# Performance work log

Measured on AMD Instinct MI355X. Metric: run time of the kernel, lower is better.

Reference implementation:

```python
import jax, jax.numpy as jnp
from jax import lax
import numpy as np

_B, _D, _H, _W = 4, 32, 256, 256   # batch, sparse grid (z,y,x)
_NPER = 50000                      # active voxels per batch element
_EPS = 1e-3                        # BatchNorm eps from norm_fn


def _subm_rulebook(coords, D, H, W):
    # gather/scatter index pairs for a 3x3x3 submanifold conv (spconv rulebook)
    N = coords.shape[0]
    b, z, y, x = coords.T
    keys = ((b * D + z) * H + y) * W + x
    order = np.argsort(keys)
    sk = keys[order]
    rin, rout = [], []
    for dz in (-1, 0, 1):
        for dy in (-1, 0, 1):
            for dx in (-1, 0, 1):
                nz, ny, nx = z + dz, y + dy, x + dx
                valid = (nz >= 0) & (nz < D) & (ny >= 0) & (ny < H) & (nx >= 0) & (nx < W)
                qk = ((b * D + nz) * H + ny) * W + nx
                pos = np.clip(np.searchsorted(sk, qk), 0, N - 1)
                found = valid & (sk[pos] == qk)
                rin.append(order[pos[found]].astype(np.int32))
                rout.append(np.nonzero(found)[0].astype(np.int32))
    P = max(len(a) for a in rin)
    Ia = np.full((27, P), N, np.int32)   # sentinel N -> zero-padded row
    Oa = np.full((27, P), N, np.int32)
    for k in range(27):
        Ia[k, :len(rin[k])] = rin[k]
        Oa[k, :len(rout[k])] = rout[k]
    return Ia, Oa


def _build():
    rng = np.random.default_rng(0)
    coords = []
    for b in range(_B):
        lin = rng.choice(_D * _H * _W, _NPER, replace=False)
        z = lin // (_H * _W); y = (lin // _W) % _H; x = lin % _W
        coords.append(np.stack([np.full(_NPER, b), z, y, x], 1))
    coords = np.concatenate(coords).astype(np.int64)
    N = coords.shape[0]
    rb1_in, rb1_out = _subm_rulebook(coords, _D, _H, _W)
    # strided SparseConv3d (k=3, s=2, p=1) rulebook + output coord set
    Do, Ho, Wo = (_D - 1) // 2 + 1, (_H - 1) // 2 + 1, (_W - 1) // 2 + 1
    b, z, y, x = coords.T
    cin, ck, ckey = [], [], []
    k = 0
    for dz in range(3):
        for dy in range(3):
            for dx in range(3):
                oz2, oy2, ox2 = z + 1 - dz, y + 1 - dy, x + 1 - dx
                valid = (oz2 % 2 == 0) & (oy2 % 2 == 0) & (ox2 % 2 == 0)
                oz, oy, ox = oz2 // 2, oy2 // 2, ox2 // 2
                valid &= (oz >= 0) & (oz < Do) & (oy >= 0) & (oy < Ho) & (ox >= 0) & (ox < Wo)
                idx = np.nonzero(valid)[0]
                cin.append(idx)
                ck.append(np.full(len(idx), k))
                ckey.append(((b[idx] * Do + oz[idx]) * Ho + oy[idx]) * Wo + ox[idx])
                k += 1
    allkey = np.concatenate(ckey)
    ukeys, inv = np.unique(allkey, return_inverse=True)
    N2 = len(ukeys)
    cin = np.concatenate(cin); ck = np.concatenate(ck)
    Pd = max(int((ck == kk).sum()) for kk in range(27))
    Id = np.full((27, Pd), N, np.int32)
    Od = np.full((27, Pd), N2, np.int32)
    for kk in range(27):
        m = ck == kk; n = int(m.sum())
        Id[kk, :n] = cin[m]; Od[kk, :n] = inv[m]
    ox = ukeys % Wo; oy = (ukeys // Wo) % Ho
    oz = (ukeys // (Wo * Ho)) % Do; ob = ukeys // (Wo * Ho * Do)
    coords2 = np.stack([ob, oz, oy, ox], 1)
    rb2_in, rb2_out = _subm_rulebook(coords2, Do, Ho, Wo)
    return N, N2, rb1_in, rb1_out, Id, Od, rb2_in, rb2_out


def setup_inputs():
    N, N2, rb1_in, rb1_out, rbd_in, rbd_out, rb2_in, rb2_out = _build()
    ks = jax.random.split(jax.random.key(0), 8)
    Cin, C0, C1 = 5, 16, 32
    return dict(
        voxel_features=jax.random.normal(ks[0], (N, Cin), jnp.float32),
        W_in=jax.random.normal(ks[1], (27, Cin, C0), jnp.float32) * 0.1,
        g_in=jnp.ones(C0), b_in=jnp.zeros(C0),
        Wb1=jax.random.normal(ks[2], (2, 2, 27, C0, C0), jnp.float32) * 0.05,
        bb1=jnp.zeros((2, 2, C0)), gb1=jnp.ones((2, 2, C0)), beb1=jnp.zeros((2, 2, C0)),
        Wp=jax.random.normal(ks[3], (27, C0, 1), jnp.float32) * 0.05,
        Wd=jax.random.normal(ks[4], (27, C0, C1), jnp.float32) * 0.05,
        g_d=jnp.ones(C1), b_d=jnp.zeros(C1),
        Wb2=jax.random.normal(ks[5], (2, 2, 27, C1, C1), jnp.float32) * 0.05,
        bb2=jnp.zeros((2, 2, C1)), gb2=jnp.ones((2, 2, C1)), beb2=jnp.zeros((2, 2, C1)),
        rb1_in=jnp.asarray(rb1_in), rb1_out=jnp.asarray(rb1_out),
        rbd_in=jnp.asarray(rbd_in), rbd_out=jnp.asarray(rbd_out),
        rb2_in=jnp.asarray(rb2_in), rb2_out=jnp.asarray(rb2_out),
        n2=int(N2),
    )


def _sparse_conv(feat, W, rin, rout, nout):
    # rulebook gather-matmul-scatter; fixed 27-iteration loop over kernel offsets
    featp = jnp.concatenate([feat, jnp.zeros((1, feat.shape[1]), feat.dtype)], 0)
    out = jnp.zeros((nout + 1, W.shape[-1]), feat.dtype)
    for k in range(W.shape[0]):
        out = out.at[rout[k]].add(featp[rin[k]] @ W[k])
    return out[:nout]


def _bn(x, g, b):
    # training-mode BatchNorm1d over active voxels (eps=1e-3)
    m = x.mean(0)
    v = ((x - m) ** 2).mean(0)
    return g * (x - m) * lax.rsqrt(v + _EPS) + b


def _basic_block(feat, Wb, bb, gb, beb, rin, rout, n):
    out = _sparse_conv(feat, Wb[0], rin, rout, n) + bb[0]
    out = jax.nn.relu(_bn(out, gb[0], beb[0]))
    out = _sparse_conv(out, Wb[1], rin, rout, n) + bb[1]
    out = _bn(out, gb[1], beb[1])
    return jax.nn.relu(out + feat)


def _forward(voxel_features, W_in, g_in, b_in, Wb1, bb1, gb1, beb1, Wp, Wd, g_d, b_d,
             Wb2, bb2, gb2, beb2, rb1_in, rb1_out, rbd_in, rbd_out, rb2_in, rb2_out, n2):
    n1 = voxel_features.shape[0]
    # conv_input: SubMConv3d + BN + ReLU
    x = jax.nn.relu(_bn(_sparse_conv(voxel_features, W_in, rb1_in, rb1_out, n1), g_in, b_in))
    for i in range(2):
        x = _basic_block(x, Wb1[i], bb1[i], gb1[i], beb1[i], rb1_in, rb1_out, n1)
    # DynamicFocalPruningDownsample: learnable importance -> topk keep (1-0.5)
    imp = jax.nn.sigmoid(_sparse_conv(x, Wp, rb1_in, rb1_out, n1))[:, 0]
    x = x * imp[:, None]
    kkeep = n1 - n1 // 2
    kth = lax.top_k(imp, kkeep)[0][-1]
    x = jnp.where(imp[:, None] >= kth, x, jnp.zeros_like(x))
    # strided SparseConv3d 16->32 + BN + ReLU
    x2 = jax.nn.relu(_bn(_sparse_conv(x, Wd, rbd_in, rbd_out, n2), g_d, b_d))
    for i in range(2):
        x2 = _basic_block(x2, Wb2[i], bb2[i], gb2[i], beb2[i], rb2_in, rb2_out, n2)
    return x2


def reference(voxel_features, W_in, g_in, b_in, Wb1, bb1, gb1, beb1, Wp, Wd, g_d, b_d,
              Wb2, bb2, gb2, beb2, rb1_in, rb1_out, rbd_in, rbd_out, rb2_in, rb2_out, n2):
    return _forward(voxel_features, W_in, g_in, b_in, Wb1, bb1, gb1, beb1, Wp, Wd, g_d, b_d,
                    Wb2, bb2, gb2, beb2, rb1_in, rb1_out, rbd_in, rbd_out, rb2_in, rb2_out, n2)
```

## Files before the change

kernel.cpp:

```cpp
#include <hip/hip_runtime.h>


typedef __attribute__((ext_vector_type(8))) short bf16x8;
typedef __attribute__((ext_vector_type(4))) float f32x4;

static __device__ __forceinline__ unsigned f2bfu(float x) {
    unsigned b = __float_as_uint(x);
    return (b + 0x7FFFu + ((b >> 16) & 1u)) >> 16;
}
static __device__ __forceinline__ float bf2f(unsigned short u) {
    return __uint_as_float(((unsigned)u) << 16);
}
static __device__ __forceinline__ int xcd_swz(int bid, int nwg) {
    if (nwg < 16) return bid;
    int q = nwg >> 3, r = nwg & 7;
    int x = bid & 7, i = bid >> 3;
    return (x < r ? x * (q + 1) : r * (q + 1) + (x - r) * q) + i;
}

__global__ void rb_count_kernel(const int* __restrict__ rout, int P, int n_out,
                                int* __restrict__ cnt) {
    int k = threadIdx.x;
    if (k >= 27) return;
    const int* r = rout + (size_t)k * P;
    int lo = 0, hi = P;
    while (lo < hi) {
        int mid = (lo + hi) >> 1;
        if (r[mid] < n_out) lo = mid + 1; else hi = mid;
    }
    cnt[k] = lo;
}

__global__ void seg_build(const int* __restrict__ rout, const int* __restrict__ cnt,
                          int P, int nb, int gran, int* __restrict__ segs) {
    const int k = blockIdx.y;
    const int b = blockIdx.x * 256 + threadIdx.x;
    if (b > nb) return;
    const int target = b * gran;
    const int* r = rout + (size_t)k * P;
    int lo = 0, hi = cnt[k];
    while (lo < hi) {
        int m = (lo + hi) >> 1;
        if (r[m] < target) lo = m + 1; else hi = m;
    }
    segs[k * (nb + 1) + b] = lo;
}

__global__ void inv_build(const int* __restrict__ rin, const int* __restrict__ rout,
                          const int* __restrict__ cnt, int P, int n_out,
                          int* __restrict__ inv) {
    const int k = blockIdx.y;
    const int p = blockIdx.x * 256 + threadIdx.x;
    if (p < cnt[k])
        inv[(size_t)k * n_out + rout[(size_t)k * P + p]] = rin[(size_t)k * P + p];
}

__global__ void prepack_w(const float* __restrict__ W, int T, int CI, int S,
                          short* __restrict__ pack) {
    int idx = blockIdx.x * 256 + threadIdx.x;
    if (idx >= S * 128) return;
    int l = idx & 63, h = (idx >> 6) & 1, s = idx >> 7;
    int co = (l & 15) + 16 * h;
#pragma unroll
    for (int j = 0; j < 8; j++) {
        int gk = s * 32 + (l >> 4) * 8 + j;
        int tap = gk / CI, cin = gk % CI;
        float w = (tap < T) ? W[((size_t)tap * CI + cin) * 32 + co] : 0.f;
        pack[(size_t)idx * 8 + j] = (short)f2bfu(w);
    }
}

template <bool OUT_BF16>
__global__ __launch_bounds__(256) void conv_mfma_sorted32(
        const unsigned short* __restrict__ feat, const short* __restrict__ Bp,
        const int* __restrict__ rin, const int* __restrict__ rout,
        const int* __restrict__ segs, int P, int nb16, int n_out,
        void* __restrict__ outv, float* __restrict__ stats) {
    __shared__ int invw[64];
    __shared__ float part[2][4][32];
    const int t = threadIdx.x, wv = t >> 6, lane = t & 63;
    const int row = lane & 15, grp = lane >> 4;
    const int bid = xcd_swz(blockIdx.x, gridDim.x);
    float ss0 = 0.f, qq0 = 0.f, ss1 = 0.f, qq1 = 0.f;

    for (int tile = 0; tile < 4; ++tile) {
        const int rowbase = bid * 256 + wv * 64 + tile * 16;
        if (rowbase >= n_out) break;
        const int tix = rowbase >> 4;
        int segv = 0;
        if (lane < 28)      segv = segs[lane * (nb16 + 1) + tix];
        else if (lane < 56) segv = segs[(lane - 28) * (nb16 + 1) + tix + 1];
        f32x4 d0 = {0.f, 0.f, 0.f, 0.f}, d1 = {0.f, 0.f, 0.f, 0.f};
        for (int k = 0; k < 27; ++k) {
            const int s0 = __shfl(segv, k);
            const int s1 = __shfl(segv, 28 + k);
            if (s0 == s1) continue;
            if (lane < 16) invw[wv * 16 + lane] = -1;
            const int e = s0 + lane;
            if (lane < 16 && e < s1)
                invw[wv * 16 + (rout[(size_t)k * P + e] - rowbase)] = rin[(size_t)k * P + e];
            asm volatile("s_waitcnt lgkmcnt(0)" ::: "memory");
            const int rn = invw[wv * 16 + row];
            union { int u[4]; bf16x8 v; } ua;
            ua.u[0] = ua.u[1] = ua.u[2] = ua.u[3] = 0;
            if (rn >= 0)
                ua.v = *(const bf16x8*)(feat + (size_t)rn * 32 + grp * 8);
            const bf16x8 b0 = *(const bf16x8*)(Bp + ((size_t)(2 * k) * 64 + lane) * 8);
            const bf16x8 b1 = *(const bf16x8*)(Bp + ((size_t)(2 * k + 1) * 64 + lane) * 8);
            d0 = __builtin_amdgcn_mfma_f32_16x16x32_bf16(ua.v, b0, d0, 0, 0, 0);
            d1 = __builtin_amdgcn_mfma_f32_16x16x32_bf16(ua.v, b1, d1, 0, 0, 0);
        }
        const int m0 = rowbase + grp * 4;
#pragma unroll
        for (int i = 0; i < 4; i++) {
            if (m0 + i < n_out) {
                if (OUT_BF16) {
                    unsigned short* o = (unsigned short*)outv;
                    o[(size_t)(m0 + i) * 32 + row]      = (unsigned short)f2bfu(d0[i]);
                    o[(size_t)(m0 + i) * 32 + row + 16] = (unsigned short)f2bfu(d1[i]);
                } else {
                    float* o = (float*)outv;
                    o[(size_t)(m0 + i) * 32 + row]      = d0[i];
                    o[(size_t)(m0 + i) * 32 + row + 16] = d1[i];
                }
            }
            ss0 += d0[i]; qq0 += d0[i] * d0[i];
            ss1 += d1[i]; qq1 += d1[i] * d1[i];
        }
    }
#pragma unroll
    for (int d = 16; d <= 32; d <<= 1) {
        ss0 += __shfl_xor(ss0, d); qq0 += __shfl_xor(qq0, d);
        ss1 += __shfl_xor(ss1, d); qq1 += __shfl_xor(qq1, d);
    }
    if (lane < 16) {
        part[0][wv][row] = ss0; part[0][wv][row + 16] = ss1;
        part[1][wv][row] = qq0; part[1][wv][row + 16] = qq1;
    }
    __syncthreads();
    if (t < 64) {
        const int which = t >> 5, co = t & 31;
        atomicAdd(&stats[which * 32 + co],
                  part[which][0][co] + part[which][1][co] +
                  part[which][2][co] + part[which][3][co]);
    }
}

__global__ __launch_bounds__(256) void conv_mfma_inv16(
        const unsigned short* __restrict__ feat, const short* __restrict__ Bp,
        const int* __restrict__ inv, int n_out,
        unsigned short* __restrict__ out, float* __restrict__ stats) {
    __shared__ float part[2][4][32];
    const int t = threadIdx.x, wv = t >> 6, lane = t & 63;
    const int row = lane & 15, grp = lane >> 4;
    const int bid = xcd_swz(blockIdx.x, gridDim.x);
    float ss0 = 0.f, qq0 = 0.f, ss1 = 0.f, qq1 = 0.f;

    for (int tile = 0; tile < 4; ++tile) {
        const int rowbase = bid * 256 + wv * 64 + tile * 16;
        if (rowbase >= n_out) break;
        const int j = rowbase + row;
        f32x4 d0 = {0.f, 0.f, 0.f, 0.f}, d1 = {0.f, 0.f, 0.f, 0.f};
        for (int s = 0; s < 14; ++s) {
            const int tap = 2 * s + (grp >> 1);
            const int cin0 = (grp & 1) * 8;
            int rn = -1;
            if (tap < 27 && j < n_out) rn = inv[(size_t)tap * n_out + j];
            union { int u[4]; bf16x8 v; } ua;
            ua.u[0] = ua.u[1] = ua.u[2] = ua.u[3] = 0;
            if (rn >= 0)
                ua.v = *(const bf16x8*)(feat + (size_t)rn * 16 + cin0);
            const bf16x8 b0 = *(const bf16x8*)(Bp + ((size_t)(2 * s) * 64 + lane) * 8);
            const bf16x8 b1 = *(const bf16x8*)(Bp + ((size_t)(2 * s + 1) * 64 + lane) * 8);
            d0 = __builtin_amdgcn_mfma_f32_16x16x32_bf16(ua.v, b0, d0, 0, 0, 0);
            d1 = __builtin_amdgcn_mfma_f32_16x16x32_bf16(ua.v, b1, d1, 0, 0, 0);
        }
        const int m0 = rowbase + grp * 4;
#pragma unroll
        for (int i = 0; i < 4; i++) {
            if (m0 + i < n_out) {
                out[(size_t)(m0 + i) * 32 + row]      = (unsigned short)f2bfu(d0[i]);
                out[(size_t)(m0 + i) * 32 + row + 16] = (unsigned short)f2bfu(d1[i]);
            }
            ss0 += d0[i]; qq0 += d0[i] * d0[i];
            ss1 += d1[i]; qq1 += d1[i] * d1[i];
        }
    }
#pragma unroll
    for (int d = 16; d <= 32; d <<= 1) {
        ss0 += __shfl_xor(ss0, d); qq0 += __shfl_xor(qq0, d);
        ss1 += __shfl_xor(ss1, d); qq1 += __shfl_xor(qq1, d);
    }
    if (lane < 16) {
        part[0][wv][row] = ss0; part[0][wv][row + 16] = ss1;
        part[1][wv][row] = qq0; part[1][wv][row + 16] = qq1;
    }
    __syncthreads();
    if (t < 64) {
        const int which = t >> 5, co = t & 31;
        atomicAdd(&stats[which * 32 + co],
                  part[which][0][co] + part[which][1][co] +
                  part[which][2][co] + part[which][3][co]);
    }
}

template <int COUT, bool SIGMOID, bool STATS>
__global__ __launch_bounds__(256) void conv16_wave(
        const float* __restrict__ feat, const float* __restrict__ W,
        const int* __restrict__ rin, const int* __restrict__ rout,
        const int* __restrict__ segs, int P, int nb64, int n_out,
        float* __restrict__ out, float* __restrict__ stats) {
    __shared__ int invw[4 * 64];
    __shared__ float part[2][4][COUT];
    const int t = threadIdx.x, wv = t >> 6, lane = t & 63;
    const int bid = xcd_swz(blockIdx.x, gridDim.x);
    const int rowbase = bid * 256 + wv * 64;
    const bool active = rowbase < n_out;
    float acc[COUT];
#pragma unroll
    for (int co = 0; co < COUT; co++) acc[co] = 0.f;

    if (active) {
        const int tix = rowbase >> 6;
        int segv = 0;
        if (lane < 28)      segv = segs[lane * (nb64 + 1) + tix];
        else if (lane < 56) segv = segs[(lane - 28) * (nb64 + 1) + tix + 1];
        for (int k = 0; k < 27; ++k) {
            const int s0 = __shfl(segv, k);
            const int s1 = __shfl(segv, 28 + k);
            if (s0 == s1) continue;
            invw[wv * 64 + lane] = -1;
            const int e = s0 + lane;
            if (e < s1)
                invw[wv * 64 + (rout[(size_t)k * P + e] - rowbase)] = rin[(size_t)k * P + e];
            asm volatile("s_waitcnt lgkmcnt(0)" ::: "memory");
            const int rn = invw[wv * 64 + lane];
            float f[16];
#pragma unroll
            for (int ci = 0; ci < 16; ci++) f[ci] = 0.f;
            if (rn >= 0) {
                const float* fr = feat + (size_t)rn * 16;
#pragma unroll
                for (int q = 0; q < 4; q++) {
                    const float4 v = *(const float4*)(fr + 4 * q);
                    f[4 * q] = v.x; f[4 * q + 1] = v.y;
                    f[4 * q + 2] = v.z; f[4 * q + 3] = v.w;
                }
            }
            const float* __restrict__ Wk = W + k * 16 * COUT;
#pragma unroll
            for (int ci = 0; ci < 16; ci++) {
                const float fv = f[ci];
#pragma unroll
                for (int co = 0; co < COUT; co++)
                    acc[co] = fmaf(fv, Wk[ci * COUT + co], acc[co]);
            }
        }
        const int j = rowbase + lane;
        if (j < n_out) {
#pragma unroll
            for (int co = 0; co < COUT; co++) {
                float v = acc[co];
                if (SIGMOID) v = 1.f / (1.f + expf(-v));
                out[(size_t)j * COUT + co] = v;
            }
        }
    }
    if (STATS) {
#pragma unroll
        for (int co = 0; co < COUT; co++) {
            float s = acc[co], s2 = s * s;
#pragma unroll
            for (int d = 1; d < 64; d <<= 1) {
                s += __shfl_xor(s, d);
                s2 += __shfl_xor(s2, d);
            }
            if (lane == 0) { part[0][wv][co] = s; part[1][wv][co] = s2; }
        }
        __syncthreads();
        if (t < 2 * COUT) {
            const int which = t / COUT, co = t - which * COUT;
            atomicAdd(&stats[which * COUT + co],
                      part[which][0][co] + part[which][1][co] +
                      part[which][2][co] + part[which][3][co]);
        }
    }
}

template <int CIN, int COUT>
__global__ __launch_bounds__(256) void conv_gather(
        const float* __restrict__ feat, const float* __restrict__ W,
        const int* __restrict__ rin, const int* __restrict__ rout,
        const int* __restrict__ segs, int P, int n_out,
        float* __restrict__ out, float* __restrict__ stats) {
    __shared__ int2 invl[256];
    __shared__ int seg[54];
    __shared__ float part[2][4][COUT];
    const int t = threadIdx.x;
    const int bid = xcd_swz(blockIdx.x, gridDim.x);
    const int j0 = bid * 256;
    const int nb1 = gridDim.x + 1;
    if (t < 54) seg[t] = segs[(t >> 1) * nb1 + bid + (t & 1)];
    invl[t] = make_int2(-1, -1);
    float acc[COUT];
#pragma unroll
    for (int co = 0; co < COUT; co++) acc[co] = 0.f;
    __syncthreads();

    for (int k = 0; k < 27; k++) {
        const int s0 = seg[2 * k], s1 = seg[2 * k + 1];
        if (s0 == s1) continue;
        const int idx = s0 + t;
        if (idx < s1)
            invl[rout[(size_t)k * P + idx] - j0] = make_int2(k, rin[(size_t)k * P + idx]);
        __syncthreads();
        const int2 e = invl[t];
        const int in = (e.x == k) ? e.y : -1;
        __syncthreads();

        float f[CIN];
#pragma unroll
        for (int ci = 0; ci < CIN; ci++) f[ci] = 0.f;
        if (in >= 0) {
            const float* fr = feat + (size_t)in * CIN;
#pragma unroll
            for (int ci = 0; ci < CIN; ci++) f[ci] = fr[ci];
        }
        const float* __restrict__ Wk = W + k * CIN * COUT;
#pragma unroll
        for (int ci = 0; ci < CIN; ci++) {
            const float fv = f[ci];
#pragma unroll
            for (int co = 0; co < COUT; co++)
                acc[co] = fmaf(fv, Wk[ci * COUT + co], acc[co]);
        }
    }

    const int j = j0 + t;
    if (j < n_out) {
#pragma unroll
        for (int co = 0; co < COUT; co++) out[(size_t)j * COUT + co] = acc[co];
    }
    const int wv = t >> 6, lane = t & 63;
#pragma unroll
    for (int co = 0; co < COUT; co++) {
        float s = acc[co], s2 = s * s;
#pragma unroll
        for (int d = 1; d < 64; d <<= 1) {
            s += __shfl_xor(s, d);
            s2 += __shfl_xor(s2, d);
        }
        if (lane == 0) { part[0][wv][co] = s; part[1][wv][co] = s2; }
    }
    __syncthreads();
    if (t < 2 * COUT) {
        const int which = t / COUT, co = t - which * COUT;
        atomicAdd(&stats[which * COUT + co],
                  part[which][0][co] + part[which][1][co] +
                  part[which][2][co] + part[which][3][co]);
    }
}

template <int C, bool RELU>
__global__ void bn_apply(const float* __restrict__ x, const float* __restrict__ stats,
                         const float* __restrict__ gg, const float* __restrict__ bb,
                         int n, float* __restrict__ y) {
    const float nf = (float)n;
    const long long total = (long long)n * C;
    for (long long idx = (long long)blockIdx.x * blockDim.x + threadIdx.x;
         idx < total; idx += (long long)gridDim.x * blockDim.x) {
        int ch = (int)(idx & (C - 1));
        float m = stats[ch] / nf;
        float v = stats[C + ch] / nf - m * m;
        float r = rsqrtf(v + 1e-3f);
        float val = gg[ch] * (x[idx] - m) * r + bb[ch];
        if (RELU) val = fmaxf(val, 0.f);
        y[idx] = val;
    }
}

template <int C>
__global__ void bn_apply_addrelu(const float* __restrict__ x,
                                 const float* __restrict__ skip,
                                 const float* __restrict__ stats,
                                 const float* __restrict__ gg,
                                 const float* __restrict__ bb,
                                 int n, float* __restrict__ y) {
    const float nf = (float)n;
    const long long total = (long long)n * C;
    for (long long idx = (long long)blockIdx.x * blockDim.x + threadIdx.x;
         idx < total; idx += (long long)gridDim.x * blockDim.x) {
        int ch = (int)(idx & (C - 1));
        float m = stats[ch] / nf;
        float v = stats[C + ch] / nf - m * m;
        float r = rsqrtf(v + 1e-3f);
        float val = gg[ch] * (x[idx] - m) * r + bb[ch] + skip[idx];
        y[idx] = fmaxf(val, 0.f);
    }
}

template <int C>
__global__ void bn_apply_b(const unsigned short* __restrict__ x,
                           const float* __restrict__ stats,
                           const float* __restrict__ gg, const float* __restrict__ bb,
                           int n, unsigned short* __restrict__ y) {
    const float nf = (float)n;
    const long long total = (long long)n * C;
    for (long long idx = (long long)blockIdx.x * blockDim.x + threadIdx.x;
         idx < total; idx += (long long)gridDim.x * blockDim.x) {
        int ch = (int)(idx & (C - 1));
        float m = stats[ch] / nf;
        float v = stats[C + ch] / nf - m * m;
        float r = rsqrtf(v + 1e-3f);
        float val = gg[ch] * (bf2f(x[idx]) - m) * r + bb[ch];
        val = fmaxf(val, 0.f);
        y[idx] = (unsigned short)f2bfu(val);
    }
}

template <int C, bool OUT_BF16>
__global__ void bn_addrelu_sb(const float* __restrict__ x,
                              const unsigned short* __restrict__ skip,
                              const float* __restrict__ stats,
                              const float* __restrict__ gg,
                              const float* __restrict__ bb,
                              int n, void* __restrict__ yv) {
    const float nf = (float)n;
    const long long total = (long long)n * C;
    for (long long idx = (long long)blockIdx.x * blockDim.x + threadIdx.x;
         idx < total; idx += (long long)gridDim.x * blockDim.x) {
        int ch = (int)(idx & (C - 1));
        float m = stats[ch] / nf;
        float v = stats[C + ch] / nf - m * m;
        float r = rsqrtf(v + 1e-3f);
        float val = gg[ch] * (x[idx] - m) * r + bb[ch] + bf2f(skip[idx]);
        val = fmaxf(val, 0.f);
        if (OUT_BF16) ((unsigned short*)yv)[idx] = (unsigned short)f2bfu(val);
        else          ((float*)yv)[idx] = val;
    }
}

__global__ __launch_bounds__(256) void hist_pass(const float* __restrict__ imp, int n,
                                                 int pass, const int* __restrict__ state,
                                                 int* __restrict__ hist) {
    __shared__ int lh[256];
    const int t = threadIdx.x;
    lh[t] = 0;
    __syncthreads();
    const int shift = 24 - 8 * pass;
    unsigned prefix = 0;
    if (pass > 0) prefix = (unsigned)state[0];
    for (int i = blockIdx.x * 256 + t; i < n; i += gridDim.x * 256) {
        unsigned u = __float_as_uint(imp[i]);
        if (pass == 0 || (u >> (shift + 8)) == prefix)
            atomicAdd(&lh[(u >> shift) & 0xFFu], 1);
    }
    __syncthreads();
    if (lh[t]) atomicAdd(&hist[pass * 256 + t], lh[t]);
}

__global__ __launch_bounds__(256) void scan_byte(const int* __restrict__ hist,
                                                 int kkeep, int pass,
                                                 int* __restrict__ state) {
    __shared__ int h[256];
    const int t = threadIdx.x;
    h[t] = hist[pass * 256 + t];
    __syncthreads();
    if (t == 0) {
        const int target = (pass == 0) ? kkeep : state[1];
        int acc = 0; int b = 255;
        for (; b > 0; b--) {
            if (acc + h[b] >= target) break;
            acc += h[b];
        }
        unsigned prefix = (pass == 0) ? 0u : (unsigned)state[0];
        prefix = (prefix << 8) | (unsigned)b;
        state[0] = (int)prefix;
        state[1] = target - acc;
        if (pass == 3) state[2] = (int)prefix;
    }
}

__global__ void prune_mask_ab(const float* __restrict__ x, const float* __restrict__ imp,
                              const int* __restrict__ state, int n,
                              unsigned short* __restrict__ ab) {
    const unsigned K = (unsigned)state[2];
    int i = blockIdx.x * blockDim.x + threadIdx.x;
    if (i >= n) return;
    float im = imp[i];
    float mult = (__float_as_uint(im) >= K) ? im : 0.f;
#pragma unroll
    for (int c = 0; c < 16; c++)
        ab[(size_t)i * 16 + c] = (unsigned short)f2bfu(x[(size_t)i * 16 + c] * mult);
}

extern "C" void kernel_launch(void* const* d_in, const int* in_sizes, int n_in,
                              void* d_out, int out_size, void* d_ws, size_t ws_size,
                              hipStream_t stream) {
    const float* vf    = (const float*)d_in[0];
    const float* W_in  = (const float*)d_in[1];
    const float* g_in  = (const float*)d_in[2];
    const float* b_in  = (const float*)d_in[3];
    const float* Wb1   = (const float*)d_in[4];
    const float* gb1   = (const float*)d_in[6];
    const float* beb1  = (const float*)d_in[7];
    const float* Wp    = (const float*)d_in[8];
    const float* Wd    = (const float*)d_in[9];
    const float* g_d   = (const float*)d_in[10];
    const float* b_d   = (const float*)d_in[11];
    const float* Wb2   = (const float*)d_in[12];
    const float* gb2   = (const float*)d_in[14];
    const float* beb2  = (const float*)d_in[15];
    const int* rb1_in  = (const int*)d_in[16];
    const int* rb1_out = (const int*)d_in[17];
    const int* rbd_in  = (const int*)d_in[18];
    const int* rbd_out = (const int*)d_in[19];
    const int* rb2_in  = (const int*)d_in[20];
    const int* rb2_out = (const int*)d_in[21];

    const int N  = in_sizes[0] / 5;
    const int P1 = in_sizes[16] / 27;
    const int Pd = in_sizes[18] / 27;
    const int P2 = in_sizes[20] / 27;
    const int n2 = out_size / 32;
    const int kkeep = N - N / 2;

    const int gs1   = (N + 255) / 256;
    const int gm2   = (n2 + 255) / 256;
    const int nb16  = (n2 + 15) / 16;
    const int nb64  = (N + 63) / 64;
    const int gew   = 2048;

    auto pad4 = [](size_t v) { return (v + 3) & ~(size_t)3; };
    float* A     = (float*)d_ws;
    float* B     = A   + pad4((size_t)N * 16);
    float* imp   = B   + pad4((size_t)N * 16);
    float* FI    = imp + pad4((size_t)N);
    float* Dbf   = FI  + pad4((size_t)n2 * 32);
    float* Ebf   = Dbf + pad4((size_t)n2 * 16);
    float* stats = Ebf + pad4((size_t)n2 * 16);
    int*   cnt1  = (int*)(stats + 64);
    int*   cntd  = cnt1 + 32;
    int*   cnt2  = cntd + 32;
    int*   hist4 = cnt2 + 32;
    int*   state = hist4 + 1024;
    int*   segs1 = state + 8;
    int*   segs64 = segs1 + 27 * (gs1 + 1);
    int*   invd   = (int*)FI;
    float* F      = FI;
    unsigned short* Ab = (unsigned short*)B;
    int*   segs16 = (int*)(B + pad4((size_t)N * 8));
    short* pack2  = (short*)imp;
    short* packd  = pack2 + 4 * 27648;
    unsigned short* Db = (unsigned short*)Dbf;
    unsigned short* Eb = (unsigned short*)Ebf;
    float* OUT   = (float*)d_out;
    float* C2    = OUT;

    rb_count_kernel<<<1, 32, 0, stream>>>(rb1_out, P1, N,  cnt1);
    rb_count_kernel<<<1, 32, 0, stream>>>(rbd_out, Pd, n2, cntd);
    rb_count_kernel<<<1, 32, 0, stream>>>(rb2_out, P2, n2, cnt2);
    seg_build<<<dim3((gs1 + 256) / 256, 27), 256, 0, stream>>>(rb1_out, cnt1, P1, gs1, 256, segs1);
    seg_build<<<dim3((nb64 + 256) / 256, 27), 256, 0, stream>>>(rb1_out, cnt1, P1, nb64, 64, segs64);

    hipMemsetAsync(stats, 0, 64 * 4, stream);
    conv_gather<5, 16><<<gs1, 256, 0, stream>>>(vf, W_in, rb1_in, rb1_out, segs1, P1, N, B, stats);
    bn_apply<16, true><<<gew, 256, 0, stream>>>(B, stats, g_in, b_in, N, A);

    for (int i = 0; i < 2; i++) {
        const float* W0 = Wb1 + (size_t)(i * 2 + 0) * 27 * 256;
        const float* W1 = Wb1 + (size_t)(i * 2 + 1) * 27 * 256;
        hipMemsetAsync(stats, 0, 64 * 4, stream);
        conv16_wave<16, false, true><<<gs1, 256, 0, stream>>>(A, W0, rb1_in, rb1_out, segs64, P1, nb64, N, B, stats);
        bn_apply<16, true><<<gew, 256, 0, stream>>>(B, stats, gb1 + (i * 2 + 0) * 16, beb1 + (i * 2 + 0) * 16, N, B);
        hipMemsetAsync(stats, 0, 64 * 4, stream);
        conv16_wave<16, false, true><<<gs1, 256, 0, stream>>>(B, W1, rb1_in, rb1_out, segs64, P1, nb64, N, C2, stats);
        bn_apply_addrelu<16><<<gew, 256, 0, stream>>>(C2, A, stats, gb1 + (i * 2 + 1) * 16, beb1 + (i * 2 + 1) * 16, N, A);
    }

    conv16_wave<1, true, false><<<gs1, 256, 0, stream>>>(A, Wp, rb1_in, rb1_out, segs64, P1, nb64, N, imp, stats);
    hipMemsetAsync(hist4, 0, 1024 * 4, stream);
    for (int p = 0; p < 4; p++) {
        hist_pass<<<128, 256, 0, stream>>>(imp, N, p, state, hist4);
        scan_byte<<<1, 256, 0, stream>>>(hist4, kkeep, p, state);
    }
    prune_mask_ab<<<(N + 255) / 256, 256, 0, stream>>>(A, imp, state, N, Ab);

    seg_build<<<dim3((nb16 + 256) / 256, 27), 256, 0, stream>>>(rb2_out, cnt2, P2, nb16, 16, segs16);
    for (int w = 0; w < 4; w++)
        prepack_w<<<14, 256, 0, stream>>>(Wb2 + (size_t)w * 27 * 1024, 27, 32, 27, pack2 + (size_t)w * 27648);
    prepack_w<<<7, 256, 0, stream>>>(Wd, 27, 16, 14, packd);
    hipMemsetAsync(invd, 0xFF, (size_t)27 * n2 * 4, stream);
    inv_build<<<dim3((Pd + 255) / 256, 27), 256, 0, stream>>>(rbd_in, rbd_out, cntd, Pd, n2, invd);

    hipMemsetAsync(stats, 0, 64 * 4, stream);
    conv_mfma_inv16<<<gm2, 256, 0, stream>>>(Ab, packd, invd, n2, Db, stats);
    bn_apply_b<32><<<gew, 256, 0, stream>>>(Db, stats, g_d, b_d, n2, Db);

    for (int i = 0; i < 2; i++) {
        const short* P0 = pack2 + (size_t)(i * 2 + 0) * 27648;
        const short* P1w = pack2 + (size_t)(i * 2 + 1) * 27648;
        hipMemsetAsync(stats, 0, 64 * 4, stream);
        conv_mfma_sorted32<true><<<gm2, 256, 0, stream>>>(Db, P0, rb2_in, rb2_out, segs16, P2, nb16, n2, Eb, stats);
        bn_apply_b<32><<<gew, 256, 0, stream>>>(Eb, stats, gb2 + (i * 2 + 0) * 32, beb2 + (i * 2 + 0) * 32, n2, Eb);
        hipMemsetAsync(stats, 0, 64 * 4, stream);
        conv_mfma_sorted32<false><<<gm2, 256, 0, stream>>>(Eb, P1w, rb2_in, rb2_out, segs16, P2, nb16, n2, F, stats);
        if (i == 0)
            bn_addrelu_sb<32, true><<<gew, 256, 0, stream>>>(F, Db, stats, gb2 + 32, beb2 + 32, n2, Db);
        else
            bn_addrelu_sb<32, false><<<gew, 256, 0, stream>>>(F, Db, stats, gb2 + 96, beb2 + 96, n2, OUT);
    }
}
```

Measured before the change: 1.282 ms.

## Replace segment-sorted rulebook gather with dense inverse index for 32ch convs

```diff
diff --git a/kernel.cpp b/kernel.cpp
--- a/kernel.cpp
+++ b/kernel.cpp
@@ -71,12 +71,10 @@
 }
 
 template <bool OUT_BF16>
-__global__ __launch_bounds__(256) void conv_mfma_sorted32(
+__global__ __launch_bounds__(256, 4) void conv_mfma_inv32(
         const unsigned short* __restrict__ feat, const short* __restrict__ Bp,
-        const int* __restrict__ rin, const int* __restrict__ rout,
-        const int* __restrict__ segs, int P, int nb16, int n_out,
+        const int* __restrict__ inv, int n_out,
         void* __restrict__ outv, float* __restrict__ stats) {
-    __shared__ int invw[64];
     __shared__ float part[2][4][32];
     const int t = threadIdx.x, wv = t >> 6, lane = t & 63;
     const int row = lane & 15, grp = lane >> 4;
@@ -86,21 +84,12 @@
     for (int tile = 0; tile < 4; ++tile) {
         const int rowbase = bid * 256 + wv * 64 + tile * 16;
         if (rowbase >= n_out) break;
-        const int tix = rowbase >> 4;
-        int segv = 0;
-        if (lane < 28)      segv = segs[lane * (nb16 + 1) + tix];
-        else if (lane < 56) segv = segs[(lane - 28) * (nb16 + 1) + tix + 1];
+        const int j = rowbase + row;
+        const bool jv = j < n_out;
         f32x4 d0 = {0.f, 0.f, 0.f, 0.f}, d1 = {0.f, 0.f, 0.f, 0.f};
+#pragma unroll
         for (int k = 0; k < 27; ++k) {
-            const int s0 = __shfl(segv, k);
-            const int s1 = __shfl(segv, 28 + k);
-            if (s0 == s1) continue;
-            if (lane < 16) invw[wv * 16 + lane] = -1;
-            const int e = s0 + lane;
-            if (lane < 16 && e < s1)
-                invw[wv * 16 + (rout[(size_t)k * P + e] - rowbase)] = rin[(size_t)k * P + e];
-            asm volatile("s_waitcnt lgkmcnt(0)" ::: "memory");
-            const int rn = invw[wv * 16 + row];
+            const int rn = jv ? inv[(size_t)k * n_out + j] : -1;
             union { int u[4]; bf16x8 v; } ua;
             ua.u[0] = ua.u[1] = ua.u[2] = ua.u[3] = 0;
             if (rn >= 0)
@@ -146,7 +135,7 @@
     }
 }
 
-__global__ __launch_bounds__(256) void conv_mfma_inv16(
+__global__ __launch_bounds__(256, 4) void conv_mfma_inv16(
         const unsigned short* __restrict__ feat, const short* __restrict__ Bp,
         const int* __restrict__ inv, int n_out,
         unsigned short* __restrict__ out, float* __restrict__ stats) {
@@ -160,12 +149,14 @@
         const int rowbase = bid * 256 + wv * 64 + tile * 16;
         if (rowbase >= n_out) break;
         const int j = rowbase + row;
+        const bool jv = j < n_out;
         f32x4 d0 = {0.f, 0.f, 0.f, 0.f}, d1 = {0.f, 0.f, 0.f, 0.f};
+#pragma unroll
         for (int s = 0; s < 14; ++s) {
             const int tap = 2 * s + (grp >> 1);
             const int cin0 = (grp & 1) * 8;
             int rn = -1;
-            if (tap < 27 && j < n_out) rn = inv[(size_t)tap * n_out + j];
+            if (tap < 27 && jv) rn = inv[(size_t)tap * n_out + j];
             union { int u[4]; bf16x8 v; } ua;
             ua.u[0] = ua.u[1] = ua.u[2] = ua.u[3] = 0;
             if (rn >= 0)
@@ -418,13 +409,13 @@
     }
 }
 
-template <int C, bool OUT_BF16>
-__global__ void bn_addrelu_sb(const float* __restrict__ x,
-                              const unsigned short* __restrict__ skip,
-                              const float* __restrict__ stats,
-                              const float* __restrict__ gg,
-                              const float* __restrict__ bb,
-                              int n, void* __restrict__ yv) {
+template <int C, bool XBF16, bool OUT_BF16>
+__global__ void bn_addrelu_x(const void* __restrict__ xv,
+                             const unsigned short* __restrict__ skip,
+                             const float* __restrict__ stats,
+                             const float* __restrict__ gg,
+                             const float* __restrict__ bb,
+                             int n, void* __restrict__ yv) {
     const float nf = (float)n;
     const long long total = (long long)n * C;
     for (long long idx = (long long)blockIdx.x * blockDim.x + threadIdx.x;
@@ -433,7 +424,9 @@
         float m = stats[ch] / nf;
         float v = stats[C + ch] / nf - m * m;
         float r = rsqrtf(v + 1e-3f);
-        float val = gg[ch] * (x[idx] - m) * r + bb[ch] + bf2f(skip[idx]);
+        float x = XBF16 ? bf2f(((const unsigned short*)xv)[idx])
+                        : ((const float*)xv)[idx];
+        float val = gg[ch] * (x - m) * r + bb[ch] + bf2f(skip[idx]);
         val = fmaxf(val, 0.f);
         if (OUT_BF16) ((unsigned short*)yv)[idx] = (unsigned short)f2bfu(val);
         else          ((float*)yv)[idx] = val;
@@ -527,7 +520,6 @@
 
     const int gs1   = (N + 255) / 256;
     const int gm2   = (n2 + 255) / 256;
-    const int nb16  = (n2 + 15) / 16;
     const int nb64  = (N + 63) / 64;
     const int gew   = 2048;
 
@@ -535,8 +527,8 @@
     float* A     = (float*)d_ws;
     float* B     = A   + pad4((size_t)N * 16);
     float* imp   = B   + pad4((size_t)N * 16);
-    float* FI    = imp + pad4((size_t)N);
-    float* Dbf   = FI  + pad4((size_t)n2 * 32);
+    float* INVf  = imp + pad4((size_t)N);
+    float* Dbf   = INVf + pad4((size_t)n2 * 27);
     float* Ebf   = Dbf + pad4((size_t)n2 * 16);
     float* stats = Ebf + pad4((size_t)n2 * 16);
     int*   cnt1  = (int*)(stats + 64);
@@ -546,15 +538,14 @@
     int*   state = hist4 + 1024;
     int*   segs1 = state + 8;
     int*   segs64 = segs1 + 27 * (gs1 + 1);
-    int*   invd   = (int*)FI;
-    float* F      = FI;
+    int*   INV    = (int*)INVf;
     unsigned short* Ab = (unsigned short*)B;
-    int*   segs16 = (int*)(B + pad4((size_t)N * 8));
     short* pack2  = (short*)imp;
     short* packd  = pack2 + 4 * 27648;
     unsigned short* Db = (unsigned short*)Dbf;
     unsigned short* Eb = (unsigned short*)Ebf;
     float* OUT   = (float*)d_out;
+    unsigned short* OUTb = (unsigned short*)d_out;
     float* C2    = OUT;
 
     rb_count_kernel<<<1, 32, 0, stream>>>(rb1_out, P1, N,  cnt1);
@@ -586,28 +577,32 @@
     }
     prune_mask_ab<<<(N + 255) / 256, 256, 0, stream>>>(A, imp, state, N, Ab);
 
-    seg_build<<<dim3((nb16 + 256) / 256, 27), 256, 0, stream>>>(rb2_out, cnt2, P2, nb16, 16, segs16);
     for (int w = 0; w < 4; w++)
         prepack_w<<<14, 256, 0, stream>>>(Wb2 + (size_t)w * 27 * 1024, 27, 32, 27, pack2 + (size_t)w * 27648);
     prepack_w<<<7, 256, 0, stream>>>(Wd, 27, 16, 14, packd);
-    hipMemsetAsync(invd, 0xFF, (size_t)27 * n2 * 4, stream);
-    inv_build<<<dim3((Pd + 255) / 256, 27), 256, 0, stream>>>(rbd_in, rbd_out, cntd, Pd, n2, invd);
+    hipMemsetAsync(INV, 0xFF, (size_t)27 * n2 * 4, stream);
+    inv_build<<<dim3((Pd + 255) / 256, 27), 256, 0, stream>>>(rbd_in, rbd_out, cntd, Pd, n2, INV);
 
     hipMemsetAsync(stats, 0, 64 * 4, stream);
-    conv_mfma_inv16<<<gm2, 256, 0, stream>>>(Ab, packd, invd, n2, Db, stats);
+    conv_mfma_inv16<<<gm2, 256, 0, stream>>>(Ab, packd, INV, n2, Db, stats);
     bn_apply_b<32><<<gew, 256, 0, stream>>>(Db, stats, g_d, b_d, n2, Db);
+
+    hipMemsetAsync(INV, 0xFF, (size_t)27 * n2 * 4, stream);
+    inv_build<<<dim3((P2 + 255) / 256, 27), 256, 0, stream>>>(rb2_in, rb2_out, cnt2, P2, n2, INV);
 
     for (int i = 0; i < 2; i++) {
         const short* P0 = pack2 + (size_t)(i * 2 + 0) * 27648;
         const short* P1w = pack2 + (size_t)(i * 2 + 1) * 27648;
         hipMemsetAsync(stats, 0, 64 * 4, stream);
-        conv_mfma_sorted32<true><<<gm2, 256, 0, stream>>>(Db, P0, rb2_in, rb2_out, segs16, P2, nb16, n2, Eb, stats);
+        conv_mfma_inv32<true><<<gm2, 256, 0, stream>>>(Db, P0, INV, n2, Eb, stats);
         bn_apply_b<32><<<gew, 256, 0, stream>>>(Eb, stats, gb2 + (i * 2 + 0) * 32, beb2 + (i * 2 + 0) * 32, n2, Eb);
         hipMemsetAsync(stats, 0, 64 * 4, stream);
-        conv_mfma_sorted32<false><<<gm2, 256, 0, stream>>>(Eb, P1w, rb2_in, rb2_out, segs16, P2, nb16, n2, F, stats);
-        if (i == 0)
-            bn_addrelu_sb<32, true><<<gew, 256, 0, stream>>>(F, Db, stats, gb2 + 32, beb2 + 32, n2, Db);
-        else
-            bn_addrelu_sb<32, false><<<gew, 256, 0, stream>>>(F, Db, stats, gb2 + 96, beb2 + 96, n2, OUT);
-    }
-}
+        if (i == 0) {
+            conv_mfma_inv32<true><<<gm2, 256, 0, stream>>>(Eb, P1w, INV, n2, OUTb, stats);
+            bn_addrelu_x<32, true, true><<<gew, 256, 0, stream>>>(OUTb, Db, stats, gb2 + 32, beb2 + 32, n2, Db);
+        } else {
+            conv_mfma_inv32<false><<<gm2, 256, 0, stream>>>(Eb, P1w, INV, n2, OUT, stats);
+            bn_addrelu_x<32, false, false><<<gew, 256, 0, stream>>>(OUT, Db, stats, gb2 + 96, beb2 + 96, n2, OUT);
+        }
+    }
+}
```

Result: slower. 1.580 ms (+23.2%).
